# Performance work log

Measured on AMD Instinct MI355X. Metric: run time of the kernel, lower is better.

Reference implementation:

```python
import jax, jax.numpy as jnp
import numpy as np

OUT_SL = 32


def gru_cell(x, h, Wih, Whh, bih, bhh):
    # PyTorch GRU cell: gates ordered (r, z, n)
    gi = x @ Wih.T + bih
    gh = h @ Whh.T + bhh
    ir, iz, inn = jnp.split(gi, 3, axis=-1)
    hr, hz, hn = jnp.split(gh, 3, axis=-1)
    r = jax.nn.sigmoid(ir + hr)
    z = jax.nn.sigmoid(iz + hz)
    n = jnp.tanh(inn + r * hn)
    return (1.0 - z) * n + z * h


def run_gru_layer(xs, h0, Wih, Whh, bih, bhh, reverse=False):
    def step(h, x):
        h = gru_cell(x, h, Wih, Whh, bih, bhh)
        return h, h
    hT, ys = jax.lax.scan(step, h0, xs, reverse=reverse)
    return ys, hT


def setup_inputs() -> dict:
    key = jax.random.key(0)
    ks = iter(jax.random.split(key, 32))

    def p(shape, fan_in):
        return (jax.random.normal(next(ks), shape, dtype=jnp.float32)
                / np.sqrt(fan_in).astype(np.float32))

    V_ENC, V_DEC, EE, ED, NH = 32000, 32000, 300, 300, 256
    inp = jax.random.randint(next(ks), (128, 64), 0, V_ENC)
    return {
        'emb_enc': p((V_ENC, EE), 1.0),
        'enc_Wih0': p((2, 3 * NH, EE), EE),
        'enc_Whh0': p((2, 3 * NH, NH), NH),
        'enc_bih0': p((2, 3 * NH), NH),
        'enc_bhh0': p((2, 3 * NH), NH),
        'enc_Wih1': p((2, 3 * NH, 2 * NH), 2 * NH),
        'enc_Whh1': p((2, 3 * NH, NH), NH),
        'enc_bih1': p((2, 3 * NH), NH),
        'enc_bhh1': p((2, 3 * NH), NH),
        'W_out_enc': p((ED, 2 * NH), 2 * NH),
        'emb_dec': p((V_DEC, ED), 1.0),
        'dec_Wih': p((2, 3 * ED, ED), ED),
        'dec_Whh': p((2, 3 * ED, ED), ED),
        'dec_bih': p((2, 3 * ED), ED),
        'dec_bhh': p((2, 3 * ED), ED),
        'W1': p((2 * NH, ED), 2 * NH),
        'l2_W': p((ED, ED), ED),
        'l2_b': p((ED,), ED),
        'l3_W': p((ED, ED + 2 * NH), ED + 2 * NH),
        'l3_b': p((ED,), ED),
        'V_att': p((ED,), ED),
        'out_b': p((V_DEC,), ED),
        'inp': inp,
    }


def reference(emb_enc, enc_Wih0, enc_Whh0, enc_bih0, enc_bhh0,
              enc_Wih1, enc_Whh1, enc_bih1, enc_bhh1, W_out_enc,
              emb_dec, dec_Wih, dec_Whh, dec_bih, dec_bhh,
              W1, l2_W, l2_b, l3_W, l3_b, V_att, out_b, inp):
    sl, bs = inp.shape
    nh = enc_Whh0.shape[-1]
    h0 = jnp.zeros((bs, nh), dtype=emb_enc.dtype)

    # ---- encoder: 2-layer bidirectional GRU (dropout in eval mode = identity)
    emb = emb_enc[inp]                                        # (sl, bs, EE)
    yf0, hf0 = run_gru_layer(emb, h0, enc_Wih0[0], enc_Whh0[0], enc_bih0[0], enc_bhh0[0])
    yb0, hb0 = run_gru_layer(emb, h0, enc_Wih0[1], enc_Whh0[1], enc_bih0[1], enc_bhh0[1], reverse=True)
    x1 = jnp.concatenate([yf0, yb0], axis=-1)                 # (sl, bs, 2*nh)
    yf1, hf1 = run_gru_layer(x1, h0, enc_Wih1[0], enc_Whh1[0], enc_bih1[0], enc_bhh1[0])
    yb1, hb1 = run_gru_layer(x1, h0, enc_Wih1[1], enc_Whh1[1], enc_bih1[1], enc_bhh1[1], reverse=True)
    enc_out = jnp.concatenate([yf1, yb1], axis=-1)            # (sl, bs, 2*nh)

    # h.view(2,2,bs,-1).permute(0,2,1,3) -> concat fwd/bwd per layer
    h = jnp.stack([jnp.concatenate([hf0, hb0], axis=-1),
                   jnp.concatenate([hf1, hb1], axis=-1)])     # (2, bs, 2*nh)
    h = h @ W_out_enc.T                                       # (2, bs, ED)

    w1e = enc_out @ W1                                        # (sl, bs, ED)
    dec_inp0 = jnp.zeros((bs,), dtype=jnp.int32)

    def dec_step(carry, _):
        h, dec_inp = carry
        w2h = h[-1] @ l2_W.T + l2_b                           # (bs, ED)
        u = jnp.tanh(w1e + w2h[None])                         # (sl, bs, ED)
        a = jax.nn.softmax(u @ V_att, axis=0)                 # (sl, bs), softmax over seq
        Xa = jnp.einsum('sb,sbd->bd', a, enc_out)             # (bs, 2*nh)
        e = emb_dec[dec_inp]                                  # (bs, ED)
        x = jnp.concatenate([e, Xa], axis=1) @ l3_W.T + l3_b  # (bs, ED)
        h0n = gru_cell(x, h[0], dec_Wih[0], dec_Whh[0], dec_bih[0], dec_bhh[0])
        h1n = gru_cell(h0n, h[1], dec_Wih[1], dec_Whh[1], dec_bih[1], dec_bhh[1])
        outp = h1n @ emb_dec.T + out_b                        # (bs, V_dec), tied weights
        ndec = jnp.argmax(outp, axis=1).astype(jnp.int32)
        return (jnp.stack([h0n, h1n]), ndec), outp

    (_, _), res = jax.lax.scan(dec_step, (h, dec_inp0), None, length=OUT_SL)
    return res                                                # (out_sl, bs, V_dec)
```

## Files before the change

kernel.cpp:

```cpp
#include <hip/hip_runtime.h>
#include <math.h>


#define DINL static __device__ __forceinline__

DINL float sigm(float x) { return 1.0f / (1.0f + expf(-x)); }
DINL float dot4f(float4 a, float4 b) { return a.x*b.x + a.y*b.y + a.z*b.z + a.w*b.w; }

DINL unsigned long long packmax(float x, int v) {
  unsigned u = __float_as_uint(x);
  u = (u & 0x80000000u) ? ~u : (u | 0x80000000u);
  return ((unsigned long long)u << 32) | (unsigned)(~v);
}
DINL unsigned long long umax64(unsigned long long a, unsigned long long b) {
  return a > b ? a : b;
}

DINL void flagbar(int* flags, int selfid, int n, int target, int tid) {
  __syncthreads();
  if (tid == 0)
    __hip_atomic_store(&flags[selfid * 32], target, __ATOMIC_RELEASE, __HIP_MEMORY_SCOPE_AGENT);
  for (int i = tid; i < n; i += 256) {
    while (__hip_atomic_load(&flags[i * 32], __ATOMIC_ACQUIRE, __HIP_MEMORY_SCOPE_AGENT) < target)
      __builtin_amdgcn_s_sleep(1);
  }
  __syncthreads();
}

__global__ __launch_bounds__(256) void k_embed(const float4* __restrict__ E,
                                               const int* __restrict__ inp,
                                               float4* __restrict__ out) {
  int i = blockIdx.x * 256 + threadIdx.x;
  if (i >= 8192 * 75) return;
  int row = i / 75, q = i - row * 75;
  out[i] = E[(size_t)inp[row] * 75 + q];
}

__global__ __launch_bounds__(256) void k_transpose(const float* __restrict__ A,
                                                   float* __restrict__ B, int R, int C) {
  __shared__ float tile[32][33];
  int c0 = blockIdx.x * 32, r0 = blockIdx.y * 32;
  int tx = threadIdx.x & 31, ty = threadIdx.x >> 5;
  for (int i = 0; i < 32; i += 8) {
    int r = r0 + ty + i, c = c0 + tx;
    if (r < R && c < C) tile[ty + i][tx] = A[(size_t)r * C + c];
  }
  __syncthreads();
  for (int i = 0; i < 32; i += 8) {
    int c = c0 + ty + i, r = r0 + tx;
    if (c < C && r < R) B[(size_t)c * R + r] = tile[tx][ty + i];
  }
}

__global__ __launch_bounds__(256) void k_gemm128(const float* __restrict__ A,
                                                 const float* __restrict__ B,
                                                 const float* __restrict__ bias,
                                                 float* __restrict__ C,
                                                 int N, int M, int K) {
  __shared__ float As[8][132];
  __shared__ float Bs[8][132];
  const int tid = threadIdx.x;
  const int bn = blockIdx.x * 128, bm = blockIdx.y * 128;
  const int tn = (tid >> 4) << 3, tm = (tid & 15) << 3;
  const int r = tid & 127;
  const bool isB = tid >= 128;
  const float* src = isB ? (B + (size_t)(bm + r) * K) : (A + (size_t)(bn + r) * K);
  const bool rowok = isB ? (bm + r < M) : (bn + r < N);
  float acc[8][8] = {};
  for (int k0 = 0; k0 < K; k0 += 8) {
    float v[8];
    if (rowok && k0 + 8 <= K) {
      float4 p0 = *(const float4*)(src + k0);
      float4 p1 = *(const float4*)(src + k0 + 4);
      v[0]=p0.x; v[1]=p0.y; v[2]=p0.z; v[3]=p0.w;
      v[4]=p1.x; v[5]=p1.y; v[6]=p1.z; v[7]=p1.w;
    } else {
#pragma unroll
      for (int j = 0; j < 8; ++j) v[j] = (rowok && k0 + j < K) ? src[k0 + j] : 0.0f;
    }
    float (*dst)[132] = isB ? Bs : As;
#pragma unroll
    for (int j = 0; j < 8; ++j) dst[j][r] = v[j];
    __syncthreads();
#pragma unroll
    for (int kk = 0; kk < 8; ++kk) {
      float a[8], b[8];
      *(float4*)&a[0] = *(const float4*)&As[kk][tn];
      *(float4*)&a[4] = *(const float4*)&As[kk][tn + 4];
      *(float4*)&b[0] = *(const float4*)&Bs[kk][tm];
      *(float4*)&b[4] = *(const float4*)&Bs[kk][tm + 4];
#pragma unroll
      for (int i = 0; i < 8; ++i)
#pragma unroll
        for (int j = 0; j < 8; ++j) acc[i][j] += a[i] * b[j];
    }
    __syncthreads();
  }
#pragma unroll
  for (int i = 0; i < 8; ++i) {
    int row = bn + tn + i;
    if (row >= N) continue;
#pragma unroll
    for (int j = 0; j < 8; ++j) {
      int col = bm + tm + j;
      if (col < M) C[(size_t)row * M + col] = acc[i][j] + (bias ? bias[col] : 0.0f);
    }
  }
}

__global__ __launch_bounds__(256) void k_enc_layer(
    const float* __restrict__ giF, const float* __restrict__ giB,
    const float* __restrict__ Whh,
    const float* __restrict__ bhh,
    float* __restrict__ y,
    float* __restrict__ hbuf,
    int* __restrict__ flags) {
  const int dir = blockIdx.z;
  const int c0 = blockIdx.x << 4;
  const int b0 = blockIdx.y << 3;
  const int tid = threadIdx.x;
  const int cl = tid >> 4;
  const int bl = (tid >> 1) & 7;
  const int ks = tid & 1;
  const float* gi = dir ? giB : giF;
  const float* W = Whh + (size_t)dir * 196608;
  const float* bh = bhh + dir * 768;
  float* hb = hbuf + dir * 16384;
  int* myflags = flags + ((dir << 3) + blockIdx.y) * 16 * 32;

  __shared__ __align__(16) float W0[16][260], W1[16][260], W2[16][260];
  __shared__ __align__(16) float hsh[8][260];

  for (int i = tid; i < 48 * 64; i += 256) {
    int row = i >> 6, q = i & 63;
    int g = row >> 4, rc = row & 15;
    float4 w = ((const float4*)W)[(size_t)(c0 + rc + (g << 8)) * 64 + q];
    float* dst = (g == 0) ? &W0[rc][0] : ((g == 1) ? &W1[rc][0] : &W2[rc][0]);
    *(float4*)&dst[q << 2] = w;
  }
  __syncthreads();

  const int b = b0 + bl, c = c0 + cl;
  const float bhr = bh[c], bhz = bh[256 + c], bhn = bh[512 + c];
  const int kbase = ks << 7;

  {
    const int tt0 = dir ? 127 : 0;
    const float* gp = gi + (size_t)tt0 * 49152 + (size_t)b * 768;
    float gr0 = gp[c], gz0 = gp[256 + c], gn0 = gp[512 + c];
    float gr = gr0, gz = gz0, gn = gn0;

    for (int t = 0; t < 128; ++t) {
      const int pp = t & 1;
      {
        const float* hsrc = hb + pp * 32768 + (b0 << 8);
        int i0 = tid, b1 = i0 >> 6, k1 = i0 & 63;
        int i1 = tid + 256, b2 = i1 >> 6, k2 = i1 & 63;
        float4 h0 = *(const float4*)(hsrc + (b1 << 8) + (k1 << 2));
        float4 h1 = *(const float4*)(hsrc + (b2 << 8) + (k2 << 2));
        *(float4*)&hsh[b1][k1 << 2] = h0;
        *(float4*)&hsh[b2][k2 << 2] = h1;
      }
      __syncthreads();

      float nr = 0.f, nz = 0.f, nn = 0.f;
      if (t < 127) {
        const int tn_ = dir ? 126 - t : t + 1;
        const float* gp2 = gi + (size_t)tn_ * 49152 + (size_t)b * 768;
        nr = gp2[c]; nz = gp2[256 + c]; nn = gp2[512 + c];
      }

      float ar = 0.f, az = 0.f, an = 0.f;
#pragma unroll 8
      for (int kq = 0; kq < 32; ++kq) {
        const int k = kbase + (kq << 2);
        float4 hv = *(const float4*)&hsh[bl][k];
        ar += dot4f(hv, *(const float4*)&W0[cl][k]);
        az += dot4f(hv, *(const float4*)&W1[cl][k]);
        an += dot4f(hv, *(const float4*)&W2[cl][k]);
      }
      ar += __shfl_xor(ar, 1);
      az += __shfl_xor(az, 1);
      an += __shfl_xor(an, 1);

      float rg = sigm(gr + ar + bhr);
      float zg = sigm(gz + az + bhz);
      float ng = tanhf(gn + rg * (an + bhn));
      float hnew = (1.f - zg) * ng + zg * hsh[bl][c];

      if (ks == 0) {
        const int tt = dir ? 127 - t : t;
        hb[(pp ^ 1) * 32768 + (b << 8) + c] = hnew;
        y[(size_t)tt * 32768 + (b << 9) + (dir << 8) + c] = hnew;
      }
      gr = nr; gz = nz; gn = nn;

      if (t < 127) flagbar(myflags, blockIdx.x, 16, t + 1, tid);
    }
  }
}

__global__ __launch_bounds__(256) void k_hcat(const float* __restrict__ x1,
                                              const float* __restrict__ encout,
                                              float* __restrict__ hcat) {
  int i = blockIdx.x * 256 + threadIdx.x;
  int l = i >> 15, r = i & 32767, b = r >> 9, d = r & 511;
  const float* src = l ? encout : x1;
  int ts = (d < 256) ? 127 : 0;
  hcat[i] = src[((size_t)(ts << 6) + b) * 512 + d];
}

DINL void gru_phase(int cb, int tid, const float* __restrict__ xin,
                    const float* __restrict__ hin, float* __restrict__ hout,
                    float* __restrict__ houtT,
                    const float* __restrict__ Wih, const float* __restrict__ Whh,
                    const float* __restrict__ bih, const float* __restrict__ bhh,
                    float* xs, float* hs) {
  const int cchunk = cb % 19, bchunk = cb / 19;
  const int cl = tid & 15, bl = tid >> 4;
  const int c = cchunk * 16 + cl;
  const int b0 = bchunk * 16, bq = b0 + bl;
  for (int i = tid; i < 16 * 75; i += 256) {
    int row = i / 75, q = i - row * 75;
    ((float4*)(xs + row * 300))[q] = ((const float4*)(xin + (size_t)(b0 + row) * 300))[q];
    ((float4*)(hs + row * 300))[q] = ((const float4*)(hin + (size_t)(b0 + row) * 300))[q];
  }
  __syncthreads();
  if (c < 300) {
    float gir = bih[c], giz = bih[300 + c], gin = bih[600 + c];
    float ghr = bhh[c], ghz = bhh[300 + c], ghn = bhh[600 + c];
    const float4* wir = (const float4*)(Wih + (size_t)c * 300);
    const float4* wiz = (const float4*)(Wih + (size_t)(300 + c) * 300);
    const float4* win = (const float4*)(Wih + (size_t)(600 + c) * 300);
    const float4* whr = (const float4*)(Whh + (size_t)c * 300);
    const float4* whz = (const float4*)(Whh + (size_t)(300 + c) * 300);
    const float4* whn = (const float4*)(Whh + (size_t)(600 + c) * 300);
    const float4* xr = (const float4*)(xs + bl * 300);
    const float4* hr = (const float4*)(hs + bl * 300);
    for (int q = 0; q < 75; ++q) {
      float4 xv = xr[q], hv = hr[q];
      gir += dot4f(xv, wir[q]);
      giz += dot4f(xv, wiz[q]);
      gin += dot4f(xv, win[q]);
      ghr += dot4f(hv, whr[q]);
      ghz += dot4f(hv, whz[q]);
      ghn += dot4f(hv, whn[q]);
    }
    float r = sigm(gir + ghr), z = sigm(giz + ghz);
    float n = tanhf(gin + r * ghn);
    float hnew = (1.f - z) * n + z * hs[bl * 300 + c];
    hout[(size_t)bq * 300 + c] = hnew;
    if (houtT) houtT[(size_t)c * 64 + bq] = hnew;
  }
}

__global__ __launch_bounds__(256) void k_dec_step(
    const float* __restrict__ hc, float* __restrict__ hn, float* __restrict__ h1T,
    const float* __restrict__ w1e, const float* __restrict__ encout,
    const float* __restrict__ l2W, const float* __restrict__ l2b,
    const float* __restrict__ l3W, const float* __restrict__ l3b,
    const float* __restrict__ Vatt, const float* __restrict__ embdec,
    const float* __restrict__ dWih, const float* __restrict__ dWhh,
    const float* __restrict__ dbih, const float* __restrict__ dbhh,
    const unsigned long long* __restrict__ prev,
    float* __restrict__ xdec, int* __restrict__ flags, int tstep) {
  const int tid = threadIdx.x, cb = blockIdx.x;
  __shared__ __align__(16) float smem[9600];
  float* h1s = smem;
  float* w2h = smem + 304;
  float* eXa = smem + 608;
  float* aa  = smem + 1424;
  float* red = smem + 1552;
  unsigned long long* redb = (unsigned long long*)(smem + 1680);

  if (cb < 64) {
    const int b = cb;
    const float* h1 = hc + 19200;
    if (tid < 128) {
      unsigned long long m = 0ULL;
      if (prev) {
        m = prev[(size_t)tid * 64 + b];
        if (tid < 122) m = umax64(m, prev[(size_t)(tid + 128) * 64 + b]);
      }
      redb[tid] = m;
    }
    for (int i = tid; i < 300; i += 256) h1s[i] = h1[b * 300 + i];
    __syncthreads();
    for (int s = 64; s > 0; s >>= 1) {
      if (tid < s) redb[tid] = umax64(redb[tid], redb[tid + s]);
      __syncthreads();
    }
    const int ib = prev ? (int)(~(unsigned)(redb[0] & 0xFFFFFFFFULL)) : 0;

    for (int m = tid; m < 300; m += 256) {
      const float4* wr = (const float4*)(l2W + (size_t)m * 300);
      const float4* hr = (const float4*)h1s;
      float acc = l2b[m];
      for (int q = 0; q < 75; ++q) acc += dot4f(wr[q], hr[q]);
      w2h[m] = acc;
    }
    __syncthreads();

    if (tid < 128) {
      const float4* wp = (const float4*)(w1e + ((size_t)(tid << 6) + b) * 300);
      const float4* vp = (const float4*)Vatt;
      const float4* hp = (const float4*)w2h;
      float acc = 0.f;
      for (int q = 0; q < 75; ++q) {
        float4 w = wp[q], h = hp[q], v = vp[q];
        acc += tanhf(w.x + h.x) * v.x + tanhf(w.y + h.y) * v.y +
               tanhf(w.z + h.z) * v.z + tanhf(w.w + h.w) * v.w;
      }
      aa[tid] = acc;
      red[tid] = acc;
    }
    __syncthreads();
    for (int s = 64; s > 0; s >>= 1) {
      if (tid < s) red[tid] = fmaxf(red[tid], red[tid + s]);
      __syncthreads();
    }
    float mx = red[0];
    __syncthreads();
    if (tid < 128) {
      float ex = expf(aa[tid] - mx);
      aa[tid] = ex;
      red[tid] = ex;
    }
    __syncthreads();
    for (int s = 64; s > 0; s >>= 1) {
      if (tid < s) red[tid] += red[tid + s];
      __syncthreads();
    }
    float inv = 1.0f / red[0];
    __syncthreads();
    if (tid < 128) aa[tid] *= inv;
    for (int d = tid; d < 300; d += 256) eXa[d] = embdec[(size_t)ib * 300 + d];
    __syncthreads();

    for (int d = tid; d < 512; d += 256) {
      float acc = 0.f;
      for (int s = 0; s < 128; ++s) acc += aa[s] * encout[((size_t)(s << 6) + b) * 512 + d];
      eXa[300 + d] = acc;
    }
    __syncthreads();

    for (int m = tid; m < 300; m += 256) {
      const float4* wr = (const float4*)(l3W + (size_t)m * 812);
      const float4* xr = (const float4*)eXa;
      float acc = l3b[m];
      for (int q = 0; q < 203; ++q) acc += dot4f(wr[q], xr[q]);
      xdec[b * 300 + m] = acc;
    }
  }

  flagbar(flags, cb, 76, 2 * tstep + 1, tid);
  gru_phase(cb, tid, xdec, hc, hn, nullptr, dWih, dWhh, dbih, dbhh,
            smem, smem + 4800);
  flagbar(flags, cb, 76, 2 * tstep + 2, tid);
  gru_phase(cb, tid, hn, hc + 19200, hn + 19200, h1T,
            dWih + 270000, dWhh + 270000, dbih + 900, dbhh + 900,
            smem, smem + 4800);
}

__global__ __launch_bounds__(256) void k_dec_out(const float* __restrict__ embT,
                                                 const float* __restrict__ h1T,
                                                 const float* __restrict__ outb,
                                                 float* __restrict__ out,
                                                 unsigned long long* __restrict__ bests) {
  const int tid = threadIdx.x;
  const int vt = tid & 127, kh = tid >> 7;
  const int v = blockIdx.x * 128 + vt;
  __shared__ float sacc[128][65];
  float acc[64];
#pragma unroll
  for (int i = 0; i < 64; ++i) acc[i] = 0.f;
  const int kb = kh * 150;
  for (int k = kb; k < kb + 150; ++k) {
    float ev = embT[(size_t)k * 32000 + v];
    const float* h = h1T + k * 64;
#pragma unroll
    for (int i = 0; i < 64; ++i) acc[i] += ev * h[i];
  }
  if (kh) {
#pragma unroll
    for (int i = 0; i < 64; ++i) sacc[vt][i] = acc[i];
  }
  __syncthreads();
  if (!kh) {
    float bo = outb[v];
#pragma unroll
    for (int i = 0; i < 64; ++i) {
      float val = acc[i] + sacc[vt][i] + bo;
      out[(size_t)i * 32000 + v] = val;
      sacc[vt][i] = val;
    }
  }
  __syncthreads();
  if (tid < 64) {
    unsigned long long best = 0ULL;
    const int v0 = blockIdx.x * 128;
    for (int q = 0; q < 128; ++q)
      best = umax64(best, packmax(sacc[q][tid], v0 + q));
    bests[(size_t)blockIdx.x * 64 + tid] = best;
  }
}

extern "C" void kernel_launch(void* const* d_in, const int* in_sizes, int n_in,
                              void* d_out_v, int out_size, void* d_ws, size_t ws_size,
                              hipStream_t stream) {
  (void)in_sizes; (void)n_in; (void)out_size; (void)ws_size;
  const float* emb_enc = (const float*)d_in[0];
  const float* eWih0   = (const float*)d_in[1];
  const float* eWhh0   = (const float*)d_in[2];
  const float* ebih0   = (const float*)d_in[3];
  const float* ebhh0   = (const float*)d_in[4];
  const float* eWih1   = (const float*)d_in[5];
  const float* eWhh1   = (const float*)d_in[6];
  const float* ebih1   = (const float*)d_in[7];
  const float* ebhh1   = (const float*)d_in[8];
  const float* Wout    = (const float*)d_in[9];
  const float* emb_dec = (const float*)d_in[10];
  const float* dWih    = (const float*)d_in[11];
  const float* dWhh    = (const float*)d_in[12];
  const float* dbih    = (const float*)d_in[13];
  const float* dbhh    = (const float*)d_in[14];
  const float* W1      = (const float*)d_in[15];
  const float* l2W     = (const float*)d_in[16];
  const float* l2b     = (const float*)d_in[17];
  const float* l3W     = (const float*)d_in[18];
  const float* l3b     = (const float*)d_in[19];
  const float* Vatt    = (const float*)d_in[20];
  const float* outb    = (const float*)d_in[21];
  const int* inp       = (const int*)d_in[22];
  float* d_out = (float*)d_out_v;

  float* ws = (float*)d_ws;
  size_t off = 0;
  auto take = [&](size_t n) { float* p = ws + off; off += (n + 3) & ~(size_t)3; return p; };
  float* embT   = take((size_t)300 * 32000);
  float* encout = take((size_t)8192 * 512);
  float* w1e    = take((size_t)8192 * 300);
  float* W1T    = take((size_t)300 * 512);
  float* hcat   = take((size_t)128 * 512);
  float* dech   = take((size_t)2 * 2 * 64 * 300);
  float* h1T    = take((size_t)300 * 64);
  float* xdec   = take((size_t)64 * 300);
  float* hbuf   = take((size_t)2 * 2 * 64 * 256);
  unsigned long long* bests = (unsigned long long*)take((size_t)250 * 64 * 2);
  int* flags_enc = (int*)take((size_t)2 * 16 * 16 * 32);
  int* flags_dec = (int*)take((size_t)76 * 32);

  float* emb  = d_out;
  float* gi0f = emb + 2457600;
  float* gi0b = gi0f + 6291456;
  float* x1   = gi0b + 6291456;
  float* gi1f = x1 + 4194304;
  float* gi1b = gi1f + 6291456;

  hipMemsetAsync(flags_enc, 0, (2 * 16 * 16 * 32 + 76 * 32) * sizeof(int), stream);

  k_embed<<<2400, 256, 0, stream>>>((const float4*)emb_enc, inp, (float4*)emb);
  k_transpose<<<dim3(10, 16), 256, 0, stream>>>(W1, W1T, 512, 300);
  k_transpose<<<dim3(10, 1000), 256, 0, stream>>>(emb_dec, embT, 32000, 300);

  k_gemm128<<<dim3(64, 6), 256, 0, stream>>>(emb, eWih0, ebih0, gi0f, 8192, 768, 300);
  k_gemm128<<<dim3(64, 6), 256, 0, stream>>>(emb, eWih0 + 230400, ebih0 + 768, gi0b, 8192, 768, 300);
  hipMemsetAsync(hbuf, 0, 2 * 2 * 64 * 256 * sizeof(float), stream);
  k_enc_layer<<<dim3(16, 8, 2), 256, 0, stream>>>(gi0f, gi0b, eWhh0, ebhh0, x1, hbuf, flags_enc);

  k_gemm128<<<dim3(64, 6), 256, 0, stream>>>(x1, eWih1, ebih1, gi1f, 8192, 768, 512);
  k_gemm128<<<dim3(64, 6), 256, 0, stream>>>(x1, eWih1 + 393216, ebih1 + 768, gi1b, 8192, 768, 512);
  hipMemsetAsync(hbuf, 0, 2 * 2 * 64 * 256 * sizeof(float), stream);
  k_enc_layer<<<dim3(16, 8, 2), 256, 0, stream>>>(gi1f, gi1b, eWhh1, ebhh1, encout, hbuf,
                                                  flags_enc + 8192);

  k_hcat<<<256, 256, 0, stream>>>(x1, encout, hcat);
  k_gemm128<<<dim3(1, 3), 256, 0, stream>>>(hcat, Wout, nullptr, dech, 128, 300, 512);
  k_gemm128<<<dim3(64, 3), 256, 0, stream>>>(encout, W1T, nullptr, w1e, 8192, 300, 512);

  for (int t = 0; t < 32; ++t) {
    int cur = t & 1, nxt = cur ^ 1;
    float* hc = dech + cur * 38400;
    float* hn = dech + nxt * 38400;
    k_dec_step<<<76, 256, 0, stream>>>(hc, hn, h1T, w1e, encout, l2W, l2b, l3W, l3b,
                                       Vatt, emb_dec, dWih, dWhh, dbih, dbhh,
                                       t ? bests : nullptr, xdec, flags_dec, t);
    k_dec_out<<<250, 256, 0, stream>>>(embT, h1T, outb,
                                       d_out + (size_t)t * 2048000, bests);
  }
}
```

Measured before the change: 12.83 ms.

## Replace all-to-all flag barriers with counter sync and split decoder step kernels

The encoder recurrence drops its per-block flag array, where every block polled 16 flags, in favour of a single atomic counter per (dir, batch-group). Each block increments the counter after its step and thread 0 spins until it reaches 16*t. Blocks shrink to 128 threads with no k-split shuffle, and the hidden state moves through agent-scope relaxed atomics. The decoder's persistent kernel with grid-wide flag barriers becomes three separate launches per step (attention, two GRU layers), trading in-kernel spin barriers for launch overhead. The relaxed-ordering sync relies on s_waitcnt and the L2 coherence of agent-scope atomics for correctness.

```diff
diff --git a/kernel.cpp b/kernel.cpp
--- a/kernel.cpp
+++ b/kernel.cpp
@@ -14,17 +14,6 @@
 }
 DINL unsigned long long umax64(unsigned long long a, unsigned long long b) {
   return a > b ? a : b;
-}
-
-DINL void flagbar(int* flags, int selfid, int n, int target, int tid) {
-  __syncthreads();
-  if (tid == 0)
-    __hip_atomic_store(&flags[selfid * 32], target, __ATOMIC_RELEASE, __HIP_MEMORY_SCOPE_AGENT);
-  for (int i = tid; i < n; i += 256) {
-    while (__hip_atomic_load(&flags[i * 32], __ATOMIC_ACQUIRE, __HIP_MEMORY_SCOPE_AGENT) < target)
-      __builtin_amdgcn_s_sleep(1);
-  }
-  __syncthreads();
 }
 
 __global__ __launch_bounds__(256) void k_embed(const float4* __restrict__ E,
@@ -108,30 +97,28 @@
   }
 }
 
-__global__ __launch_bounds__(256) void k_enc_layer(
+__global__ __launch_bounds__(128) void k_enc_layer(
     const float* __restrict__ giF, const float* __restrict__ giB,
     const float* __restrict__ Whh,
     const float* __restrict__ bhh,
     float* __restrict__ y,
     float* __restrict__ hbuf,
-    int* __restrict__ flags) {
+    unsigned* __restrict__ flags) {
   const int dir = blockIdx.z;
   const int c0 = blockIdx.x << 4;
   const int b0 = blockIdx.y << 3;
   const int tid = threadIdx.x;
-  const int cl = tid >> 4;
-  const int bl = (tid >> 1) & 7;
-  const int ks = tid & 1;
+  const int cl = tid & 15, bl = tid >> 4;
   const float* gi = dir ? giB : giF;
   const float* W = Whh + (size_t)dir * 196608;
   const float* bh = bhh + dir * 768;
   float* hb = hbuf + dir * 16384;
-  int* myflags = flags + ((dir << 3) + blockIdx.y) * 16 * 32;
+  unsigned* flag = flags + ((dir << 3) + blockIdx.y) * 32;
 
   __shared__ __align__(16) float W0[16][260], W1[16][260], W2[16][260];
   __shared__ __align__(16) float hsh[8][260];
 
-  for (int i = tid; i < 48 * 64; i += 256) {
+  for (int i = tid; i < 48 * 64; i += 128) {
     int row = i >> 6, q = i & 63;
     int g = row >> 4, rc = row & 15;
     float4 w = ((const float4*)W)[(size_t)(c0 + rc + (g << 8)) * 64 + q];
@@ -142,61 +129,68 @@
 
   const int b = b0 + bl, c = c0 + cl;
   const float bhr = bh[c], bhz = bh[256 + c], bhn = bh[512 + c];
-  const int kbase = ks << 7;
-
+
+  float gr, gz, gn;
   {
     const int tt0 = dir ? 127 : 0;
     const float* gp = gi + (size_t)tt0 * 49152 + (size_t)b * 768;
-    float gr0 = gp[c], gz0 = gp[256 + c], gn0 = gp[512 + c];
-    float gr = gr0, gz = gz0, gn = gn0;
-
-    for (int t = 0; t < 128; ++t) {
-      const int pp = t & 1;
-      {
-        const float* hsrc = hb + pp * 32768 + (b0 << 8);
-        int i0 = tid, b1 = i0 >> 6, k1 = i0 & 63;
-        int i1 = tid + 256, b2 = i1 >> 6, k2 = i1 & 63;
-        float4 h0 = *(const float4*)(hsrc + (b1 << 8) + (k1 << 2));
-        float4 h1 = *(const float4*)(hsrc + (b2 << 8) + (k2 << 2));
-        *(float4*)&hsh[b1][k1 << 2] = h0;
-        *(float4*)&hsh[b2][k2 << 2] = h1;
+    gr = gp[c]; gz = gp[256 + c]; gn = gp[512 + c];
+  }
+
+  for (int t = 0; t < 128; ++t) {
+    if (t) {
+      if (tid == 0) {
+        while (__hip_atomic_fetch_add(flag, 0u, __ATOMIC_RELAXED,
+                                      __HIP_MEMORY_SCOPE_AGENT) < 16u * (unsigned)t)
+          __builtin_amdgcn_s_sleep(2);
       }
       __syncthreads();
-
-      float nr = 0.f, nz = 0.f, nn = 0.f;
-      if (t < 127) {
-        const int tn_ = dir ? 126 - t : t + 1;
-        const float* gp2 = gi + (size_t)tn_ * 49152 + (size_t)b * 768;
-        nr = gp2[c]; nz = gp2[256 + c]; nn = gp2[512 + c];
+    }
+    const int pp = t & 1;
+    {
+      const unsigned* hsrc = (const unsigned*)(hb + pp * 32768 + (b0 << 8));
+      for (int i = tid; i < 2048; i += 128) {
+        unsigned ub = __hip_atomic_load(hsrc + i, __ATOMIC_RELAXED,
+                                        __HIP_MEMORY_SCOPE_AGENT);
+        hsh[i >> 8][i & 255] = __uint_as_float(ub);
       }
-
-      float ar = 0.f, az = 0.f, an = 0.f;
+    }
+    __syncthreads();
+
+    float nr = 0.f, nz = 0.f, nn = 0.f;
+    if (t < 127) {
+      const int tn_ = dir ? 126 - t : t + 1;
+      const float* gp2 = gi + (size_t)tn_ * 49152 + (size_t)b * 768;
+      nr = gp2[c]; nz = gp2[256 + c]; nn = gp2[512 + c];
+    }
+
+    float ar = 0.f, az = 0.f, an = 0.f;
 #pragma unroll 8
-      for (int kq = 0; kq < 32; ++kq) {
-        const int k = kbase + (kq << 2);
-        float4 hv = *(const float4*)&hsh[bl][k];
-        ar += dot4f(hv, *(const float4*)&W0[cl][k]);
-        az += dot4f(hv, *(const float4*)&W1[cl][k]);
-        an += dot4f(hv, *(const float4*)&W2[cl][k]);
-      }
-      ar += __shfl_xor(ar, 1);
-      az += __shfl_xor(az, 1);
-      an += __shfl_xor(an, 1);
-
-      float rg = sigm(gr + ar + bhr);
-      float zg = sigm(gz + az + bhz);
-      float ng = tanhf(gn + rg * (an + bhn));
-      float hnew = (1.f - zg) * ng + zg * hsh[bl][c];
-
-      if (ks == 0) {
-        const int tt = dir ? 127 - t : t;
-        hb[(pp ^ 1) * 32768 + (b << 8) + c] = hnew;
-        y[(size_t)tt * 32768 + (b << 9) + (dir << 8) + c] = hnew;
-      }
-      gr = nr; gz = nz; gn = nn;
-
-      if (t < 127) flagbar(myflags, blockIdx.x, 16, t + 1, tid);
-    }
+    for (int kq = 0; kq < 64; ++kq) {
+      const int k = kq << 2;
+      float4 hv = *(const float4*)&hsh[bl][k];
+      ar += dot4f(hv, *(const float4*)&W0[cl][k]);
+      az += dot4f(hv, *(const float4*)&W1[cl][k]);
+      an += dot4f(hv, *(const float4*)&W2[cl][k]);
+    }
+
+    float rg = sigm(gr + ar + bhr);
+    float zg = sigm(gz + az + bhz);
+    float ng = tanhf(gn + rg * (an + bhn));
+    float hnew = (1.f - zg) * ng + zg * hsh[bl][c];
+
+    const int tt = dir ? 127 - t : t;
+    __hip_atomic_exchange((unsigned*)&hb[(pp ^ 1) * 32768 + (b << 8) + c],
+                          __float_as_uint(hnew), __ATOMIC_RELAXED,
+                          __HIP_MEMORY_SCOPE_AGENT);
+    y[(size_t)tt * 32768 + (b << 9) + (dir << 8) + c] = hnew;
+
+    asm volatile("s_waitcnt vmcnt(0)" ::: "memory");
+    __syncthreads();
+    if (t < 127 && tid == 0)
+      __hip_atomic_fetch_add(flag, 1u, __ATOMIC_RELAXED, __HIP_MEMORY_SCOPE_AGENT);
+
+    gr = nr; gz = nz; gn = nn;
   }
 }
 
@@ -210,20 +204,115 @@
   hcat[i] = src[((size_t)(ts << 6) + b) * 512 + d];
 }
 
-DINL void gru_phase(int cb, int tid, const float* __restrict__ xin,
-                    const float* __restrict__ hin, float* __restrict__ hout,
-                    float* __restrict__ houtT,
-                    const float* __restrict__ Wih, const float* __restrict__ Whh,
-                    const float* __restrict__ bih, const float* __restrict__ bhh,
-                    float* xs, float* hs) {
-  const int cchunk = cb % 19, bchunk = cb / 19;
+__global__ __launch_bounds__(256) void k_dec_att(
+    const float* __restrict__ h1, const float* __restrict__ w1e,
+    const float* __restrict__ encout,
+    const float* __restrict__ l2W, const float* __restrict__ l2b,
+    const float* __restrict__ l3W, const float* __restrict__ l3b,
+    const float* __restrict__ Vatt, const float* __restrict__ embdec,
+    const unsigned long long* __restrict__ prev,
+    float* __restrict__ xdec) {
+  const int b = blockIdx.x, tid = threadIdx.x;
+  __shared__ __align__(16) float h1s[304];
+  __shared__ __align__(16) float w2h[304];
+  __shared__ __align__(16) float eXa[816];
+  __shared__ float aa[128];
+  __shared__ float red[128];
+  __shared__ unsigned long long redb[128];
+
+  if (tid < 128) {
+    unsigned long long m = 0ULL;
+    if (prev) {
+      m = prev[(size_t)tid * 64 + b];
+      if (tid < 122) m = umax64(m, prev[(size_t)(tid + 128) * 64 + b]);
+    }
+    redb[tid] = m;
+  }
+  for (int i = tid; i < 300; i += 256) h1s[i] = h1[b * 300 + i];
+  __syncthreads();
+  for (int s = 64; s > 0; s >>= 1) {
+    if (tid < s) redb[tid] = umax64(redb[tid], redb[tid + s]);
+    __syncthreads();
+  }
+  const int ib = prev ? (int)(~(unsigned)(redb[0] & 0xFFFFFFFFULL)) : 0;
+
+  for (int m = tid; m < 300; m += 256) {
+    const float4* wr = (const float4*)(l2W + (size_t)m * 300);
+    const float4* hr = (const float4*)h1s;
+    float acc = l2b[m];
+    for (int q = 0; q < 75; ++q) acc += dot4f(wr[q], hr[q]);
+    w2h[m] = acc;
+  }
+  __syncthreads();
+
+  if (tid < 128) {
+    const float4* wp = (const float4*)(w1e + ((size_t)(tid << 6) + b) * 300);
+    const float4* vp = (const float4*)Vatt;
+    const float4* hp = (const float4*)w2h;
+    float acc = 0.f;
+    for (int q = 0; q < 75; ++q) {
+      float4 w = wp[q], h = hp[q], v = vp[q];
+      acc += tanhf(w.x + h.x) * v.x + tanhf(w.y + h.y) * v.y +
+             tanhf(w.z + h.z) * v.z + tanhf(w.w + h.w) * v.w;
+    }
+    aa[tid] = acc;
+    red[tid] = acc;
+  }
+  __syncthreads();
+  for (int s = 64; s > 0; s >>= 1) {
+    if (tid < s) red[tid] = fmaxf(red[tid], red[tid + s]);
+    __syncthreads();
+  }
+  float mx = red[0];
+  __syncthreads();
+  if (tid < 128) {
+    float ex = expf(aa[tid] - mx);
+    aa[tid] = ex;
+    red[tid] = ex;
+  }
+  __syncthreads();
+  for (int s = 64; s > 0; s >>= 1) {
+    if (tid < s) red[tid] += red[tid + s];
+    __syncthreads();
+  }
+  float inv = 1.0f / red[0];
+  __syncthreads();
+  if (tid < 128) aa[tid] *= inv;
+  for (int d = tid; d < 300; d += 256) eXa[d] = embdec[(size_t)ib * 300 + d];
+  __syncthreads();
+
+  for (int d = tid; d < 512; d += 256) {
+    float acc = 0.f;
+    for (int s = 0; s < 128; ++s) acc += aa[s] * encout[((size_t)(s << 6) + b) * 512 + d];
+    eXa[300 + d] = acc;
+  }
+  __syncthreads();
+
+  for (int m = tid; m < 300; m += 256) {
+    const float4* wr = (const float4*)(l3W + (size_t)m * 812);
+    const float4* xr = (const float4*)eXa;
+    float acc = l3b[m];
+    for (int q = 0; q < 203; ++q) acc += dot4f(wr[q], xr[q]);
+    xdec[b * 300 + m] = acc;
+  }
+}
+
+__global__ __launch_bounds__(256) void k_gru300(
+    const float* __restrict__ xin, const float* __restrict__ hin,
+    float* __restrict__ hout, float* __restrict__ houtT,
+    const float* __restrict__ Wih, const float* __restrict__ Whh,
+    const float* __restrict__ bih, const float* __restrict__ bhh) {
+  const int tid = threadIdx.x;
   const int cl = tid & 15, bl = tid >> 4;
-  const int c = cchunk * 16 + cl;
-  const int b0 = bchunk * 16, bq = b0 + bl;
+  const int c = blockIdx.x * 16 + cl;
+  const int b0 = blockIdx.y * 16;
+  const int b = b0 + bl;
+  __shared__ __align__(16) float xs[16][300];
+  __shared__ __align__(16) float hs[16][300];
   for (int i = tid; i < 16 * 75; i += 256) {
     int row = i / 75, q = i - row * 75;
-    ((float4*)(xs + row * 300))[q] = ((const float4*)(xin + (size_t)(b0 + row) * 300))[q];
-    ((float4*)(hs + row * 300))[q] = ((const float4*)(hin + (size_t)(b0 + row) * 300))[q];
+    ((float4*)&xs[row][0])[q] = ((const float4*)(xin + (size_t)(b0 + row) * 300))[q];
+    ((float4*)&hs[row][0])[q] = ((const float4*)(hin + (size_t)(b0 + row) * 300))[q];
   }
   __syncthreads();
   if (c < 300) {
@@ -235,8 +324,8 @@
     const float4* whr = (const float4*)(Whh + (size_t)c * 300);
     const float4* whz = (const float4*)(Whh + (size_t)(300 + c) * 300);
     const float4* whn = (const float4*)(Whh + (size_t)(600 + c) * 300);
-    const float4* xr = (const float4*)(xs + bl * 300);
-    const float4* hr = (const float4*)(hs + bl * 300);
+    const float4* xr = (const float4*)&xs[bl][0];
+    const float4* hr = (const float4*)&hs[bl][0];
     for (int q = 0; q < 75; ++q) {
       float4 xv = xr[q], hv = hr[q];
       gir += dot4f(xv, wir[q]);
@@ -248,118 +337,10 @@
     }
     float r = sigm(gir + ghr), z = sigm(giz + ghz);
     float n = tanhf(gin + r * ghn);
-    float hnew = (1.f - z) * n + z * hs[bl * 300 + c];
-    hout[(size_t)bq * 300 + c] = hnew;
-    if (houtT) houtT[(size_t)c * 64 + bq] = hnew;
-  }
-}
-
-__global__ __launch_bounds__(256) void k_dec_step(
-    const float* __restrict__ hc, float* __restrict__ hn, float* __restrict__ h1T,
-    const float* __restrict__ w1e, const float* __restrict__ encout,
-    const float* __restrict__ l2W, const float* __restrict__ l2b,
-    const float* __restrict__ l3W, const float* __restrict__ l3b,
-    const float* __restrict__ Vatt, const float* __restrict__ embdec,
-    const float* __restrict__ dWih, const float* __restrict__ dWhh,
-    const float* __restrict__ dbih, const float* __restrict__ dbhh,
-    const unsigned long long* __restrict__ prev,
-    float* __restrict__ xdec, int* __restrict__ flags, int tstep) {
-  const int tid = threadIdx.x, cb = blockIdx.x;
-  __shared__ __align__(16) float smem[9600];
-  float* h1s = smem;
-  float* w2h = smem + 304;
-  float* eXa = smem + 608;
-  float* aa  = smem + 1424;
-  float* red = smem + 1552;
-  unsigned long long* redb = (unsigned long long*)(smem + 1680);
-
-  if (cb < 64) {
-    const int b = cb;
-    const float* h1 = hc + 19200;
-    if (tid < 128) {
-      unsigned long long m = 0ULL;
-      if (prev) {
-        m = prev[(size_t)tid * 64 + b];
-        if (tid < 122) m = umax64(m, prev[(size_t)(tid + 128) * 64 + b]);
-      }
-      redb[tid] = m;
-    }
-    for (int i = tid; i < 300; i += 256) h1s[i] = h1[b * 300 + i];
-    __syncthreads();
-    for (int s = 64; s > 0; s >>= 1) {
-      if (tid < s) redb[tid] = umax64(redb[tid], redb[tid + s]);
-      __syncthreads();
-    }
-    const int ib = prev ? (int)(~(unsigned)(redb[0] & 0xFFFFFFFFULL)) : 0;
-
-    for (int m = tid; m < 300; m += 256) {
-      const float4* wr = (const float4*)(l2W + (size_t)m * 300);
-      const float4* hr = (const float4*)h1s;
-      float acc = l2b[m];
-      for (int q = 0; q < 75; ++q) acc += dot4f(wr[q], hr[q]);
-      w2h[m] = acc;
-    }
-    __syncthreads();
-
-    if (tid < 128) {
-      const float4* wp = (const float4*)(w1e + ((size_t)(tid << 6) + b) * 300);
-      const float4* vp = (const float4*)Vatt;
-      const float4* hp = (const float4*)w2h;
-      float acc = 0.f;
-      for (int q = 0; q < 75; ++q) {
-        float4 w = wp[q], h = hp[q], v = vp[q];
-        acc += tanhf(w.x + h.x) * v.x + tanhf(w.y + h.y) * v.y +
-               tanhf(w.z + h.z) * v.z + tanhf(w.w + h.w) * v.w;
-      }
-      aa[tid] = acc;
-      red[tid] = acc;
-    }
-    __syncthreads();
-    for (int s = 64; s > 0; s >>= 1) {
-      if (tid < s) red[tid] = fmaxf(red[tid], red[tid + s]);
-      __syncthreads();
-    }
-    float mx = red[0];
-    __syncthreads();
-    if (tid < 128) {
-      float ex = expf(aa[tid] - mx);
-      aa[tid] = ex;
-      red[tid] = ex;
-    }
-    __syncthreads();
-    for (int s = 64; s > 0; s >>= 1) {
-      if (tid < s) red[tid] += red[tid + s];
-      __syncthreads();
-    }
-    float inv = 1.0f / red[0];
-    __syncthreads();
-    if (tid < 128) aa[tid] *= inv;
-    for (int d = tid; d < 300; d += 256) eXa[d] = embdec[(size_t)ib * 300 + d];
-    __syncthreads();
-
-    for (int d = tid; d < 512; d += 256) {
-      float acc = 0.f;
-      for (int s = 0; s < 128; ++s) acc += aa[s] * encout[((size_t)(s << 6) + b) * 512 + d];
-      eXa[300 + d] = acc;
-    }
-    __syncthreads();
-
-    for (int m = tid; m < 300; m += 256) {
-      const float4* wr = (const float4*)(l3W + (size_t)m * 812);
-      const float4* xr = (const float4*)eXa;
-      float acc = l3b[m];
-      for (int q = 0; q < 203; ++q) acc += dot4f(wr[q], xr[q]);
-      xdec[b * 300 + m] = acc;
-    }
-  }
-
-  flagbar(flags, cb, 76, 2 * tstep + 1, tid);
-  gru_phase(cb, tid, xdec, hc, hn, nullptr, dWih, dWhh, dbih, dbhh,
-            smem, smem + 4800);
-  flagbar(flags, cb, 76, 2 * tstep + 2, tid);
-  gru_phase(cb, tid, hn, hc + 19200, hn + 19200, h1T,
-            dWih + 270000, dWhh + 270000, dbih + 900, dbhh + 900,
-            smem, smem + 4800);
+    float hnew = (1.f - z) * n + z * hs[bl][c];
+    hout[(size_t)b * 300 + c] = hnew;
+    if (houtT) houtT[(size_t)c * 64 + b] = hnew;
+  }
 }
 
 __global__ __launch_bounds__(256) void k_dec_out(const float* __restrict__ embT,
@@ -447,8 +428,7 @@
   float* xdec   = take((size_t)64 * 300);
   float* hbuf   = take((size_t)2 * 2 * 64 * 256);
   unsigned long long* bests = (unsigned long long*)take((size_t)250 * 64 * 2);
-  int* flags_enc = (int*)take((size_t)2 * 16 * 16 * 32);
-  int* flags_dec = (int*)take((size_t)76 * 32);
+  unsigned* flags = (unsigned*)take((size_t)2 * 16 * 32);
 
   float* emb  = d_out;
   float* gi0f = emb + 2457600;
@@ -457,7 +437,7 @@
   float* gi1f = x1 + 4194304;
   float* gi1b = gi1f + 6291456;
 
-  hipMemsetAsync(flags_enc, 0, (2 * 16 * 16 * 32 + 76 * 32) * sizeof(int), stream);
+  hipMemsetAsync(flags, 0, 2 * 16 * 32 * sizeof(unsigned), stream);
 
   k_embed<<<2400, 256, 0, stream>>>((const float4*)emb_enc, inp, (float4*)emb);
   k_transpose<<<dim3(10, 16), 256, 0, stream>>>(W1, W1T, 512, 300);
@@ -466,13 +446,13 @@
   k_gemm128<<<dim3(64, 6), 256, 0, stream>>>(emb, eWih0, ebih0, gi0f, 8192, 768, 300);
   k_gemm128<<<dim3(64, 6), 256, 0, stream>>>(emb, eWih0 + 230400, ebih0 + 768, gi0b, 8192, 768, 300);
   hipMemsetAsync(hbuf, 0, 2 * 2 * 64 * 256 * sizeof(float), stream);
-  k_enc_layer<<<dim3(16, 8, 2), 256, 0, stream>>>(gi0f, gi0b, eWhh0, ebhh0, x1, hbuf, flags_enc);
+  k_enc_layer<<<dim3(16, 8, 2), 128, 0, stream>>>(gi0f, gi0b, eWhh0, ebhh0, x1, hbuf, flags);
 
   k_gemm128<<<dim3(64, 6), 256, 0, stream>>>(x1, eWih1, ebih1, gi1f, 8192, 768, 512);
   k_gemm128<<<dim3(64, 6), 256, 0, stream>>>(x1, eWih1 + 393216, ebih1 + 768, gi1b, 8192, 768, 512);
   hipMemsetAsync(hbuf, 0, 2 * 2 * 64 * 256 * sizeof(float), stream);
-  k_enc_layer<<<dim3(16, 8, 2), 256, 0, stream>>>(gi1f, gi1b, eWhh1, ebhh1, encout, hbuf,
-                                                  flags_enc + 8192);
+  k_enc_layer<<<dim3(16, 8, 2), 128, 0, stream>>>(gi1f, gi1b, eWhh1, ebhh1, encout, hbuf,
+                                                  flags + 512);
 
   k_hcat<<<256, 256, 0, stream>>>(x1, encout, hcat);
   k_gemm128<<<dim3(1, 3), 256, 0, stream>>>(hcat, Wout, nullptr, dech, 128, 300, 512);
@@ -482,9 +462,13 @@
     int cur = t & 1, nxt = cur ^ 1;
     float* hc = dech + cur * 38400;
     float* hn = dech + nxt * 38400;
-    k_dec_step<<<76, 256, 0, stream>>>(hc, hn, h1T, w1e, encout, l2W, l2b, l3W, l3b,
-                                       Vatt, emb_dec, dWih, dWhh, dbih, dbhh,
-                                       t ? bests : nullptr, xdec, flags_dec, t);
+    k_dec_att<<<64, 256, 0, stream>>>(hc + 19200, w1e, encout, l2W, l2b, l3W, l3b,
+                                      Vatt, emb_dec, t ? bests : nullptr, xdec);
+    k_gru300<<<dim3(19, 4), 256, 0, stream>>>(xdec, hc, hn, nullptr,
+                                              dWih, dWhh, dbih, dbhh);
+    k_gru300<<<dim3(19, 4), 256, 0, stream>>>(hn, hc + 19200, hn + 19200, h1T,
+                                              dWih + 270000, dWhh + 270000,
+                                              dbih + 900, dbhh + 900);
     k_dec_out<<<250, 256, 0, stream>>>(embT, h1T, outb,
                                        d_out + (size_t)t * 2048000, bests);
   }
```

Result: faster. 11.64 ms (-9.2%).
